# Kernel tuning notes

Measured on AMD Instinct MI355X. Metric: run time of the kernel, lower is better.

## Reference

```python
import jax, jax.numpy as jnp
import numpy as np

C = 32
C_Z = 128
S = 256
N_SEQ = 256
LN_EPS = 1e-5


def setup_inputs() -> dict:
    key = jax.random.key(0)
    k1, k2, k3, k4 = jax.random.split(key, 4)
    m_si = jax.random.normal(k1, (S, N_SEQ, C), dtype=jnp.float32)
    ln_gamma = jnp.ones((C,), dtype=jnp.float32)
    ln_beta = jnp.zeros((C,), dtype=jnp.float32)
    # nn.Linear(c, 2c, bias=False): weight shape (2c, c)
    W_ab = jax.random.normal(k2, (2 * C, C), dtype=jnp.float32) / np.sqrt(C)
    # nn.Linear(c*c, c_z): weight (c_z, c*c), bias (c_z,)
    W_out = jax.random.normal(k3, (C_Z, C * C), dtype=jnp.float32) / np.sqrt(C * C)
    b_out = jax.random.normal(k4, (C_Z,), dtype=jnp.float32) * 0.01
    return {"m_si": m_si, "ln_gamma": ln_gamma, "ln_beta": ln_beta,
            "W_ab": W_ab, "W_out": W_out, "b_out": b_out}


def reference(m_si, ln_gamma, ln_beta, W_ab, W_out, b_out):
    # LayerNorm over channel dim c
    mu = jnp.mean(m_si, axis=-1, keepdims=True)
    var = jnp.var(m_si, axis=-1, keepdims=True)
    x = (m_si - mu) * jax.lax.rsqrt(var + LN_EPS) * ln_gamma + ln_beta
    # linear_no_bias then chunk into a, b: each (s, n_seq, c)
    ab = jnp.einsum('snc,dc->snd', x, W_ab)
    a, b = ab[..., :C], ab[..., C:]
    # mean over MSA sequences of outer products a[s,i,:] x b[s,j,:]
    # restructured as a contraction over n_seq: (i, j, c, c)
    outer = jnp.einsum('inc,jnd->ijcd', a, b) / N_SEQ
    outer = outer.reshape(S, S, C * C)  # flatten (c, c) -> c*c
    # final linear projection to c_z
    z_ij = jnp.einsum('ijk,zk->ijz', outer, W_out) + b_out
    return z_ij
```

## Files before the change

kernel.cpp:

```cpp
#include <hip/hip_runtime.h>

#define SDIM 256
#define NSEQ 256
#define CDIM 32
#define CZ 128
#define IB 8
#define JB 4

typedef __bf16 bfx8 __attribute__((ext_vector_type(8)));
typedef float fx4 __attribute__((ext_vector_type(4)));
typedef float f32x16 __attribute__((ext_vector_type(16)));
typedef unsigned int u32x4 __attribute__((ext_vector_type(4)));

__device__ __forceinline__ unsigned short f2bf(float f) {
  unsigned int u = __float_as_uint(f);
  u += 0x7fffu + ((u >> 16) & 1u);
  return (unsigned short)(u >> 16);
}

__device__ __forceinline__ unsigned int cvtpk(float lo, float hi) {
  unsigned int r;
  asm("v_cvt_pk_bf16_f32 %0, %1, %2" : "=v"(r) : "v"(lo), "v"(hi));
  return r;
}

__device__ __forceinline__ void gload16(const void* g, void* l) {
  __builtin_amdgcn_global_load_lds((const __attribute__((address_space(1))) unsigned int*)g,
                                   (__attribute__((address_space(3))) unsigned int*)l,
                                   16, 0, 0);
}


__global__ __launch_bounds__(256) void opm_prep(
    const float* __restrict__ m_si, const float* __restrict__ gamma, const float* __restrict__ beta,
    const float* __restrict__ Wab, const float* __restrict__ Wout,
    unsigned short* __restrict__ a_t, unsigned short* __restrict__ b_t,
    unsigned short* __restrict__ w2T)
{
  __shared__ __align__(16) char shbuf[41216];
  const int b = blockIdx.x;
  const int t = threadIdx.x;
  if (b < 2 * SDIM) {
    float* xin = (float*)shbuf;
    unsigned short* xt = (unsigned short*)shbuf;
    fx4* wab4 = (fx4*)(shbuf + 36864);
    float* gbuf = (float*)(shbuf + 36864 + 4096);
    const int s = b >> 1, dph = b & 1;

    const float* msrc = m_si + s * 8192;
#pragma unroll
    for (int k = 0; k < 8; ++k) {
      const int q = t + k * 256;
      ((fx4*)xin)[(q >> 3) * 9 + (q & 7)] = ((const fx4*)msrc)[q];
    }
    wab4[t & 255] = ((const fx4*)(Wab + dph * 1024))[t & 255];
    if (t < 32) { gbuf[t] = gamma[t]; gbuf[32 + t] = beta[t]; }
    __syncthreads();

    float x[CDIM];
#pragma unroll
    for (int c = 0; c < CDIM; ++c) x[c] = xin[t * 36 + c];
    __syncthreads();

    float mu = 0.f;
#pragma unroll
    for (int c = 0; c < CDIM; ++c) mu += x[c];
    mu *= (1.f / CDIM);
    float var = 0.f;
#pragma unroll
    for (int c = 0; c < CDIM; ++c) { float d = x[c] - mu; var += d * d; }
    var *= (1.f / CDIM);
    const float inv = rsqrtf(var + 1e-5f);
    fx4 xv[8];
#pragma unroll
    for (int cq = 0; cq < 8; ++cq) {
      fx4 v;
#pragma unroll
      for (int j = 0; j < 4; ++j) {
        const int c = cq * 4 + j;
        v[j] = (x[c] - mu) * inv * gbuf[c] + gbuf[32 + c];
      }
      xv[cq] = v;
    }

    for (int dp = 0; dp < 32; ++dp) {
      fx4 a = xv[0] * wab4[dp * 8];
#pragma unroll
      for (int cq = 1; cq < 8; ++cq) a += xv[cq] * wab4[dp * 8 + cq];
      xt[dp * 256 + t] = f2bf(a[0] + a[1] + a[2] + a[3]);
    }
    __syncthreads();

    unsigned short* outb = dph ? b_t : a_t;
#pragma unroll
    for (int k = 0; k < 4; ++k) {
      const int q = t + k * 256;
      const int row = q >> 5, cc = q & 31;
      *(u32x4*)(outb + (s * 32 + row) * 256 + cc * 8) = *(const u32x4*)(shbuf + row * 512 + cc * 16);
    }
  } else {
    unsigned short* lin = (unsigned short*)shbuf;
    const int blk = b - 2 * SDIM;
    const float* wsrc = Wout + blk * 4096;
#pragma unroll
    for (int jj = 0; jj < 4; ++jj) {
      const int q = t + jj * 256;
      const fx4 v = ((const fx4*)wsrc)[q];
      unsigned short* dst = lin + q * 4;
      dst[0] = f2bf(v[0]); dst[1] = f2bf(v[1]); dst[2] = f2bf(v[2]); dst[3] = f2bf(v[3]);
    }
    __syncthreads();
    const int z0 = blk * 4;
#pragma unroll
    for (int w = 0; w < 2; ++w) {
      const int id = t + w * 256;
      const int lz = id & 3;
      const int hh = (id >> 2) & 1;
      const int ks = id >> 3;
      const int z = z0 + lz;
      unsigned short vals[8];
#pragma unroll
      for (int e = 0; e < 8; ++e) {
        const int kp = ks * 16 + hh * 8 + e;
        const int c = (kp & 3) | (((kp >> 8) & 1) << 2) | (((kp >> 2) & 1) << 3) | (((kp >> 9) & 1) << 4);
        const int d = (kp >> 3) & 31;
        vals[e] = lin[lz * 1024 + c * CDIM + d];
      }
      const int dest = ((z >> 5) << 15) + (ks << 9) + (hh << 8) + ((z & 31) << 3);
      *(u32x4*)(w2T + dest) = *(const u32x4*)vals;
    }
  }
}

__global__ __launch_bounds__(512, 4) void opm_main(
    const unsigned short* __restrict__ a_t, const unsigned short* __restrict__ b_t,
    const unsigned short* __restrict__ w2T, const float* __restrict__ bout,
    float* __restrict__ out)
{
  __shared__ __align__(16) char smem[65536];
  char* o_sh = smem;

  const int tid = threadIdx.x;
  const int lane = tid & 63;
  const int wid = tid >> 6;
  const int l31 = lane & 31;
  const int h = lane >> 5;

  const int bxr = blockIdx.x;
  const int xc = bxr & 7;
  const int q8 = bxr >> 3;
  const int it = q8 >> 4;
  const int jt = q8 & 15;
  const int i0 = ((xc & 1) * 16 + it) * IB;
  const int j0 = ((xc >> 1) * 16 + jt) * JB;

  const int wm = wid >> 1;
  const int wn = wid & 1;
  const int wbase = wid * 1024;

  f32x16 acc00 = {}, acc01 = {}, acc10 = {}, acc11 = {};

  auto STAGE = [&](int buf, int nc) {
    const int nbase = nc * 32;
    char* A = smem + 16384 + buf * 16384;
    char* B = smem + 49152 + buf * 8192;
#pragma unroll
    for (int pass = 0; pass < 2; ++pass) {
      const int q = pass * 512 + tid;
      const int row = q >> 2;
      const int gs = (q & 3) ^ ((q >> 3) & 3);
      const unsigned short* src = a_t + ((i0 + (row >> 5)) * 32 + (row & 31)) * 256 + nbase + gs * 8;
      gload16(src, A + pass * 8192 + wbase);
    }
    {
      const int q = tid;
      const int row = q >> 2;
      const int gs = (q & 3) ^ ((q >> 3) & 3);
      const unsigned short* src = b_t + ((j0 + (row >> 5)) * 32 + (row & 31)) * 256 + nbase + gs * 8;
      gload16(src, B + wbase);
    }
  };

  auto COMPUTE = [&](int buf) {
    char* A = smem + 16384 + buf * 16384;
    char* B = smem + 49152 + buf * 8192;
#pragma unroll
    for (int ks = 0; ks < 2; ++ks) {
      const int s = ks * 2 + h;
      bfx8 af0, af1, bf0, bf1;
      { const int r = wm * 64 + l31;      af0 = *(const bfx8*)(A + r * 64 + (((s ^ (r >> 1)) & 3) << 4)); }
      { const int r = wm * 64 + 32 + l31; af1 = *(const bfx8*)(A + r * 64 + (((s ^ (r >> 1)) & 3) << 4)); }
      { const int r = wn * 64 + l31;      bf0 = *(const bfx8*)(B + r * 64 + (((s ^ (r >> 1)) & 3) << 4)); }
      { const int r = wn * 64 + 32 + l31; bf1 = *(const bfx8*)(B + r * 64 + (((s ^ (r >> 1)) & 3) << 4)); }
      __builtin_amdgcn_s_setprio(1);
      acc00 = __builtin_amdgcn_mfma_f32_32x32x16_bf16(af0, bf0, acc00, 0, 0, 0);
      acc01 = __builtin_amdgcn_mfma_f32_32x32x16_bf16(af0, bf1, acc01, 0, 0, 0);
      acc10 = __builtin_amdgcn_mfma_f32_32x32x16_bf16(af1, bf0, acc10, 0, 0, 0);
      acc11 = __builtin_amdgcn_mfma_f32_32x32x16_bf16(af1, bf1, acc11, 0, 0, 0);
      __builtin_amdgcn_s_setprio(0);
    }
  };

  STAGE(0, 0);
#pragma unroll 2
  for (int t = 0; t < 8; ++t) {
    if (t < 7) {
      STAGE((t + 1) & 1, t + 1);
      asm volatile("s_waitcnt vmcnt(3)" ::: "memory");
    } else {
      asm volatile("s_waitcnt vmcnt(0)" ::: "memory");
    }
    __builtin_amdgcn_s_barrier();
    asm volatile("" ::: "memory");
    COMPUTE(t & 1);
    asm volatile("s_waitcnt lgkmcnt(0)" ::: "memory");
    __builtin_amdgcn_s_barrier();
  }

  {
    const f32x16 av[4] = { acc00 * 0.00390625f, acc01 * 0.00390625f,
                           acc10 * 0.00390625f, acc11 * 0.00390625f };
#pragma unroll
    for (int mi = 0; mi < 2; ++mi) {
#pragma unroll
      for (int ni = 0; ni < 2; ++ni) {
        const f32x16 a = av[mi * 2 + ni];
        const int p = (wm * 2 + mi) * 4 + (wn * 2 + ni);
#pragma unroll
        for (int c4 = 0; c4 < 2; ++c4) {
          const int sl = l31 + 32 * h + 64 * c4;
          u32x4 v;
          v[0] = cvtpk(a[8 * c4 + 0], a[8 * c4 + 1]);
          v[1] = cvtpk(a[8 * c4 + 2], a[8 * c4 + 3]);
          v[2] = cvtpk(a[8 * c4 + 4], a[8 * c4 + 5]);
          v[3] = cvtpk(a[8 * c4 + 6], a[8 * c4 + 7]);
          *(u32x4*)(o_sh + p * 2048 + ((sl ^ (p & 7)) << 4)) = v;
        }
      }
    }
  }
  __syncthreads();

  {
    const int ztp = wid & 1;
    const int kh = wid >> 1;
    const unsigned short* wpa = w2T + ((ztp * 2 + 0) << 15) + (h << 8) + (l31 << 3);
    const unsigned short* wpb = w2T + ((ztp * 2 + 1) << 15) + (h << 8) + (l31 << 3);
    const int obase = l31 * 2048;
    const int oxor = l31 & 7;
    const int ks0 = kh * 16;

    bfx8 wa[4], wb[4];
#pragma unroll
    for (int q = 0; q < 4; ++q) {
      wa[q] = *(const bfx8*)(wpa + ((ks0 + q) << 9));
      wb[q] = *(const bfx8*)(wpb + ((ks0 + q) << 9));
    }
    bfx8 oc = *(const bfx8*)(o_sh + obase + ((((ks0 << 1) + h) ^ oxor) << 4));
    bfx8 on = *(const bfx8*)(o_sh + obase + (((((ks0 + 1) << 1) + h) ^ oxor) << 4));

    f32x16 za = {}, zb = {};
#pragma unroll
    for (int st = 0; st < 16; ++st) {
      const int q = st & 3;
      __builtin_amdgcn_s_setprio(1);
      za = __builtin_amdgcn_mfma_f32_32x32x16_bf16(wa[q], oc, za, 0, 0, 0);
      zb = __builtin_amdgcn_mfma_f32_32x32x16_bf16(wb[q], oc, zb, 0, 0, 0);
      __builtin_amdgcn_s_setprio(0);
      oc = on;
      if (st < 14) on = *(const bfx8*)(o_sh + obase + (((((ks0 + st + 2) << 1) + h) ^ oxor) << 4));
      if (st < 12) {
        wa[q] = *(const bfx8*)(wpa + ((ks0 + st + 4) << 9));
        wb[q] = *(const bfx8*)(wpb + ((ks0 + st + 4) << 9));
      }
    }
    __syncthreads();

    const int slot = (kh >> 1) * 2 + ztp;
    auto PWRITE = [&](char* base) {
#pragma unroll
      for (int zs = 0; zs < 2; ++zs) {
        const f32x16& A = zs ? zb : za;
#pragma unroll
        for (int g2 = 0; g2 < 4; ++g2) {
          fx4 v = { A[4 * g2], A[4 * g2 + 1], A[4 * g2 + 2], A[4 * g2 + 3] };
          *(fx4*)(base + zs * 4096 + (((g2 * 2 + h) * 32 + l31) << 4)) = v;
        }
      }
    };
    auto PADD = [&](const char* base) {
#pragma unroll
      for (int zs = 0; zs < 2; ++zs) {
        f32x16& A = zs ? zb : za;
#pragma unroll
        for (int g2 = 0; g2 < 4; ++g2) {
          const fx4 v = *(const fx4*)(base + zs * 4096 + (((g2 * 2 + h) * 32 + l31) << 4));
          A[4 * g2 + 0] += v[0]; A[4 * g2 + 1] += v[1];
          A[4 * g2 + 2] += v[2]; A[4 * g2 + 3] += v[3];
        }
      }
    };
    if (kh & 1) PWRITE(o_sh + slot * 8192);
    __syncthreads();
    if (!(kh & 1)) {
      PADD(o_sh + slot * 8192);
      if (kh == 2) PWRITE(o_sh + 32768 + ztp * 8192);
    }
    __syncthreads();
    if (kh == 0) {
      PADD(o_sh + 32768 + ztp * 8192);
      const int i = i0 + (l31 >> 2), j = j0 + (l31 & 3);
      float* op = out + (i * SDIM + j) * CZ + ztp * 64;
      const float* bp = bout + ztp * 64;
#pragma unroll
      for (int zs = 0; zs < 2; ++zs) {
        const f32x16& A = zs ? zb : za;
#pragma unroll
        for (int g2 = 0; g2 < 4; ++g2) {
          const int zl = zs * 32 + g2 * 8 + h * 4;
          fx4 v = { A[4 * g2], A[4 * g2 + 1], A[4 * g2 + 2], A[4 * g2 + 3] };
          v += *(const fx4*)(bp + zl);
          *(fx4*)(op + zl) = v;
        }
      }
    }
  }
}

extern "C" void kernel_launch(void* const* d_in, const int* in_sizes, int n_in,
                              void* d_out, int out_size, void* d_ws, size_t ws_size,
                              hipStream_t stream) {
  const float* m_si  = (const float*)d_in[0];
  const float* gamma = (const float*)d_in[1];
  const float* beta  = (const float*)d_in[2];
  const float* Wab   = (const float*)d_in[3];
  const float* Wout  = (const float*)d_in[4];
  const float* bout  = (const float*)d_in[5];
  float* out = (float*)d_out;

  char* ws = (char*)d_ws;
  unsigned short* a_t = (unsigned short*)ws;
  unsigned short* b_t = (unsigned short*)(ws + (4u << 20));
  unsigned short* w2T = (unsigned short*)(ws + (8u << 20));

  opm_prep<<<dim3(2 * SDIM + 32), dim3(256), 0, stream>>>(m_si, gamma, beta, Wab, Wout, a_t, b_t, w2T);
  opm_main<<<dim3(2048), dim3(512), 0, stream>>>(a_t, b_t, w2T, bout, out);
}
```

Measured before the change: 81.41 us.

## Compute LayerNorm+W_ab projection in prep kernel with MFMA, one block per s

Rewrites the prep kernel's LayerNorm and a/b projection so that each block handles one s with 64-lane wavefronts. LayerNorm statistics are reduced with cross-lane shuffles, and the 64x32 projection is done with bf16 16x16x32 MFMA instructions instead of scalar FMAs. This removes the large LDS staging buffer and halves the number of prep blocks, since a and b are produced together. The cost is scattered 2-byte global stores to a_t/b_t, a single-pass variance (E[x^2]-mu^2), and the input converted to bf16 before the projection, all of which may reduce accuracy slightly.

After: 77.93 us. -4.3%, faster.

```diff
diff --git a/kernel.cpp b/kernel.cpp
--- a/kernel.cpp
+++ b/kernel.cpp
@@ -24,6 +24,13 @@
   return r;
 }
 
+__device__ __forceinline__ bfx8 pack8(const fx4 lo, const fx4 hi) {
+  bfx8 r;
+  r[0] = (__bf16)lo[0]; r[1] = (__bf16)lo[1]; r[2] = (__bf16)lo[2]; r[3] = (__bf16)lo[3];
+  r[4] = (__bf16)hi[0]; r[5] = (__bf16)hi[1]; r[6] = (__bf16)hi[2]; r[7] = (__bf16)hi[3];
+  return r;
+}
+
 __device__ __forceinline__ void gload16(const void* g, void* l) {
   __builtin_amdgcn_global_load_lds((const __attribute__((address_space(1))) unsigned int*)g,
                                    (__attribute__((address_space(3))) unsigned int*)l,
@@ -37,70 +44,64 @@
     unsigned short* __restrict__ a_t, unsigned short* __restrict__ b_t,
     unsigned short* __restrict__ w2T)
 {
-  __shared__ __align__(16) char shbuf[41216];
+  __shared__ __align__(16) char shbuf[8192];
   const int b = blockIdx.x;
   const int t = threadIdx.x;
-  if (b < 2 * SDIM) {
-    float* xin = (float*)shbuf;
-    unsigned short* xt = (unsigned short*)shbuf;
-    fx4* wab4 = (fx4*)(shbuf + 36864);
-    float* gbuf = (float*)(shbuf + 36864 + 4096);
-    const int s = b >> 1, dph = b & 1;
-
-    const float* msrc = m_si + s * 8192;
-#pragma unroll
-    for (int k = 0; k < 8; ++k) {
-      const int q = t + k * 256;
-      ((fx4*)xin)[(q >> 3) * 9 + (q & 7)] = ((const fx4*)msrc)[q];
-    }
-    wab4[t & 255] = ((const fx4*)(Wab + dph * 1024))[t & 255];
-    if (t < 32) { gbuf[t] = gamma[t]; gbuf[32 + t] = beta[t]; }
-    __syncthreads();
-
-    float x[CDIM];
-#pragma unroll
-    for (int c = 0; c < CDIM; ++c) x[c] = xin[t * 36 + c];
-    __syncthreads();
-
-    float mu = 0.f;
-#pragma unroll
-    for (int c = 0; c < CDIM; ++c) mu += x[c];
-    mu *= (1.f / CDIM);
-    float var = 0.f;
-#pragma unroll
-    for (int c = 0; c < CDIM; ++c) { float d = x[c] - mu; var += d * d; }
-    var *= (1.f / CDIM);
-    const float inv = rsqrtf(var + 1e-5f);
-    fx4 xv[8];
-#pragma unroll
-    for (int cq = 0; cq < 8; ++cq) {
-      fx4 v;
-#pragma unroll
-      for (int j = 0; j < 4; ++j) {
-        const int c = cq * 4 + j;
-        v[j] = (x[c] - mu) * inv * gbuf[c] + gbuf[32 + c];
-      }
-      xv[cq] = v;
-    }
-
-    for (int dp = 0; dp < 32; ++dp) {
-      fx4 a = xv[0] * wab4[dp * 8];
-#pragma unroll
-      for (int cq = 1; cq < 8; ++cq) a += xv[cq] * wab4[dp * 8 + cq];
-      xt[dp * 256 + t] = f2bf(a[0] + a[1] + a[2] + a[3]);
-    }
-    __syncthreads();
-
-    unsigned short* outb = dph ? b_t : a_t;
-#pragma unroll
-    for (int k = 0; k < 4; ++k) {
-      const int q = t + k * 256;
-      const int row = q >> 5, cc = q & 31;
-      *(u32x4*)(outb + (s * 32 + row) * 256 + cc * 8) = *(const u32x4*)(shbuf + row * 512 + cc * 16);
+  if (b < SDIM) {
+    const int s = b;
+    const int l = t & 63;
+    const int w = t >> 6;
+    const int nl = l & 15;
+    const int cg = l >> 4;
+
+    bfx8 afr[4];
+#pragma unroll
+    for (int dt = 0; dt < 4; ++dt) {
+      const float* wr = Wab + (dt * 16 + nl) * 32 + cg * 8;
+      afr[dt] = pack8(*(const fx4*)wr, *(const fx4*)(wr + 4));
+    }
+    const fx4 g0 = *(const fx4*)(gamma + cg * 8);
+    const fx4 g1 = *(const fx4*)(gamma + cg * 8 + 4);
+    const fx4 bt0 = *(const fx4*)(beta + cg * 8);
+    const fx4 bt1 = *(const fx4*)(beta + cg * 8 + 4);
+
+#pragma unroll
+    for (int p = 0; p < 4; ++p) {
+      const int n = p * 64 + w * 16 + nl;
+      const float* xr = m_si + (s * 256 + n) * 32 + cg * 8;
+      const fx4 v0 = *(const fx4*)xr;
+      const fx4 v1 = *(const fx4*)(xr + 4);
+      float ps  = v0[0] + v0[1] + v0[2] + v0[3] + v1[0] + v1[1] + v1[2] + v1[3];
+      float ps2 = v0[0]*v0[0] + v0[1]*v0[1] + v0[2]*v0[2] + v0[3]*v0[3]
+                + v1[0]*v1[0] + v1[1]*v1[1] + v1[2]*v1[2] + v1[3]*v1[3];
+      ps  += __shfl_xor(ps, 16);  ps  += __shfl_xor(ps, 32);
+      ps2 += __shfl_xor(ps2, 16); ps2 += __shfl_xor(ps2, 32);
+      const float mu = ps * 0.03125f;
+      const float var = ps2 * 0.03125f - mu * mu;
+      const float inv = rsqrtf(var + 1e-5f);
+      const fx4 e0 = (v0 - mu) * inv * g0 + bt0;
+      const fx4 e1 = (v1 - mu) * inv * g1 + bt1;
+      const bfx8 bfr = pack8(e0, e1);
+
+      fx4 dz[4];
+#pragma unroll
+      for (int dt = 0; dt < 4; ++dt)
+        dz[dt] = __builtin_amdgcn_mfma_f32_16x16x32_bf16(afr[dt], bfr, (fx4){0.f,0.f,0.f,0.f}, 0, 0, 0);
+
+#pragma unroll
+      for (int dt = 0; dt < 4; ++dt) {
+#pragma unroll
+        for (int r = 0; r < 4; ++r) {
+          const int d = dt * 16 + cg * 4 + r;
+          const unsigned short hv = f2bf(dz[dt][r]);
+          if (d < 32) a_t[(s * 32 + d) * 256 + n] = hv;
+          else        b_t[(s * 32 + (d - 32)) * 256 + n] = hv;
+        }
+      }
     }
   } else {
     unsigned short* lin = (unsigned short*)shbuf;
-    const int blk = b - 2 * SDIM;
+    const int blk = b - SDIM;
     const float* wsrc = Wout + blk * 4096;
 #pragma unroll
     for (int jj = 0; jj < 4; ++jj) {
@@ -343,6 +344,6 @@
   unsigned short* b_t = (unsigned short*)(ws + (4u << 20));
   unsigned short* w2T = (unsigned short*)(ws + (8u << 20));
 
-  opm_prep<<<dim3(2 * SDIM + 32), dim3(256), 0, stream>>>(m_si, gamma, beta, Wab, Wout, a_t, b_t, w2T);
+  opm_prep<<<dim3(SDIM + 32), dim3(256), 0, stream>>>(m_si, gamma, beta, Wab, Wout, a_t, b_t, w2T);
   opm_main<<<dim3(2048), dim3(512), 0, stream>>>(a_t, b_t, w2T, bout, out);
 }
```
